# Optimization experiments

Measured on AMD Instinct MI355X. Metric: run time of the kernel, lower is better.

The kernel has to match this reference:

```python
import jax, jax.numpy as jnp
import numpy as np

# Config (matches init_kwargs)
L = 2        # depth
DIM = 512
H = 8        # heads
DH = 64      # dim_head
MLP = 2048
B = 4
N = 1024
BLOCK = 32   # compress / selection block size
TOPK = 8     # num_selected_blocks
WRAD = 32    # sliding window radius (window size 64)


def setup_inputs() -> dict:
    key = jax.random.key(0)
    ks = jax.random.split(key, 10)
    s = 0.02
    def rn(k, shape):
        return jax.random.normal(k, shape, dtype=jnp.float32) * s
    return {
        "x": jax.random.normal(ks[0], (B, N, DIM), dtype=jnp.float32),
        "ln1_g": jnp.ones((L, DIM), jnp.float32), "ln1_b": jnp.zeros((L, DIM), jnp.float32),
        "Wq": rn(ks[1], (L, DIM, H * DH)), "Wk": rn(ks[2], (L, DIM, H * DH)), "Wv": rn(ks[3], (L, DIM, H * DH)),
        "Wg": rn(ks[4], (L, DIM, H * 3)), "bg": jnp.zeros((L, H * 3), jnp.float32),
        "Wo": rn(ks[5], (L, H * DH, DIM)), "bo": jnp.zeros((L, DIM), jnp.float32),
        "ln2_g": jnp.ones((L, DIM), jnp.float32), "ln2_b": jnp.zeros((L, DIM), jnp.float32),
        "W1": rn(ks[6], (L, DIM, MLP)), "b1": jnp.zeros((L, MLP), jnp.float32),
        "W2": rn(ks[7], (L, MLP, DIM)), "b2": jnp.zeros((L, DIM), jnp.float32),
    }


def _ln(x, g, b):
    m = x.mean(-1, keepdims=True)
    v = jnp.var(x, axis=-1, keepdims=True)
    return (x - m) * jax.lax.rsqrt(v + 1e-5) * g + b


def _sparse_attn(x, lng, lnb, Wq, Wk, Wv, Wg, bg, Wo, bo):
    # NSA-style 3-branch attention: compressed + selected-blocks + sliding window,
    # combined with per-head sigmoid gates. Non-causal (ViT).
    b, n, _ = x.shape
    h = _ln(x, lng, lnb)
    q = (h @ Wq).reshape(b, n, H, DH).transpose(0, 2, 1, 3)  # bhnd
    k = (h @ Wk).reshape(b, n, H, DH).transpose(0, 2, 1, 3)
    v = (h @ Wv).reshape(b, n, H, DH).transpose(0, 2, 1, 3)
    q = q * (DH ** -0.5)
    nb = n // BLOCK
    # --- compressed branch: mean-pool K/V per block
    kc = k.reshape(b, H, nb, BLOCK, DH).mean(3)              # bhmd (m = nb blocks)
    vc = v.reshape(b, H, nb, BLOCK, DH).mean(3)
    sc = jnp.einsum('bhnd,bhmd->bhnm', q, kc)                # per-query block scores
    out_c = jnp.einsum('bhnm,bhmd->bhnd', jax.nn.softmax(sc, -1), vc)
    # --- selection branch: top-k blocks per query (from compressed scores)
    idx = jax.lax.top_k(sc, TOPK)[1]                         # [b,h,n,TOPK]
    blk_mask = (idx[..., :, None] == jnp.arange(nb)).any(-2) # [b,h,n,nb]
    tok_mask = jnp.repeat(blk_mask, BLOCK, axis=-1)          # [b,h,n,n]
    s = jnp.einsum('bhnd,bhmd->bhnm', q, k)                  # shared fine scores
    neg = jnp.finfo(s.dtype).min
    out_s = jnp.einsum('bhnm,bhmd->bhnd',
                       jax.nn.softmax(jnp.where(tok_mask, s, neg), -1), v)
    # --- sliding window branch
    i = jnp.arange(n)
    wmask = jnp.abs(i[:, None] - i[None, :]) <= WRAD
    out_w = jnp.einsum('bhnm,bhmd->bhnd',
                       jax.nn.softmax(jnp.where(wmask, s, neg), -1), v)
    # --- gate and combine
    gates = jax.nn.sigmoid(h @ Wg + bg).reshape(b, n, H, 3).transpose(0, 2, 1, 3)[..., None]  # [b,H,n,3,1]
    out = gates[:, :, :, 0] * out_c + gates[:, :, :, 1] * out_s + gates[:, :, :, 2] * out_w
    out = out.transpose(0, 2, 1, 3).reshape(b, n, H * DH)
    return out @ Wo + bo


def reference(x, ln1_g, ln1_b, Wq, Wk, Wv, Wg, bg, Wo, bo, ln2_g, ln2_b, W1, b1, W2, b2):
    for l in range(L):
        x = _sparse_attn(x, ln1_g[l], ln1_b[l], Wq[l], Wk[l], Wv[l],
                         Wg[l], bg[l], Wo[l], bo[l]) + x
        h = _ln(x, ln2_g[l], ln2_b[l])
        x = jax.nn.gelu(h @ W1[l] + b1[l]) @ W2[l] + b2[l] + x
    return x
```

## Files before the change

kernel.cpp:

```cpp
#include <hip/hip_runtime.h>
#include <cstdint>
#include <cstddef>

typedef __attribute__((ext_vector_type(4))) float f32x4;
typedef __attribute__((ext_vector_type(16))) float f32x16;
typedef __attribute__((ext_vector_type(8))) short short8;
typedef __attribute__((ext_vector_type(4))) short s16x4;
typedef __attribute__((ext_vector_type(2))) int int2v;
typedef unsigned short u16;

#define DEVINL static __device__ __forceinline__
#define MFMA32(A,B,C) __builtin_amdgcn_mfma_f32_32x32x16_bf16(A,B,C,0,0,0)

constexpr int NBATCH = 4;
constexpr int NSEQ   = 1024;
constexpr int NDIM   = 512;
constexpr int NHEAD  = 8;
constexpr int NDH    = 64;
constexpr int NMLP   = 2048;
constexpr int NROWS  = NBATCH * NSEQ;
constexpr int NBLKC  = 32;
constexpr int NBH    = NBATCH * NHEAD;
constexpr int NQKV   = 1664;

DEVINL float b2f(u16 u) { union { unsigned u; float f; } x; x.u = ((unsigned)u) << 16; return x.f; }
DEVINL u16 f2b(float v) {
    union { float f; unsigned u; } x; x.f = v;
    unsigned r = x.u + 0x7fff + ((x.u >> 16) & 1);
    return (u16)(r >> 16);
}
DEVINL float fastrcp(float x) { float r; asm("v_rcp_f32 %0, %1" : "=v"(r) : "v"(x)); return r; }

DEVINL void gload16(const void* g, void* l)
{
    __builtin_amdgcn_global_load_lds(
        (const __attribute__((address_space(1))) void*)g,
        (__attribute__((address_space(3))) void*)l, 16, 0, 0);
}

__global__ void __launch_bounds__(256) ln_kernel(const float* __restrict__ x,
    const float* __restrict__ gg, const float* __restrict__ bb, u16* __restrict__ out)
{
    int row = blockIdx.x * 4 + (threadIdx.x >> 6);
    int lane = threadIdx.x & 63;
    const float* xr = x + (size_t)row * NDIM + lane * 8;
    f32x4 a = *(const f32x4*)xr;
    f32x4 c = *(const f32x4*)(xr + 4);
    float xv[8] = { a[0], a[1], a[2], a[3], c[0], c[1], c[2], c[3] };
    float s = 0.f, s2 = 0.f;
    #pragma unroll
    for (int i = 0; i < 8; ++i) { s += xv[i]; s2 += xv[i] * xv[i]; }
    #pragma unroll
    for (int d = 1; d < 64; d <<= 1) { s += __shfl_xor(s, d); s2 += __shfl_xor(s2, d); }
    float mean = s * (1.f / NDIM);
    float var = s2 * (1.f / NDIM) - mean * mean;
    float rstd = rsqrtf(var + 1e-5f);
    const float* gp = gg + lane * 8;
    const float* bp = bb + lane * 8;
    short8 o;
    #pragma unroll
    for (int i = 0; i < 8; ++i)
        o[i] = (short)f2b((xv[i] - mean) * rstd * gp[i] + bp[i]);
    *(short8*)(out + (size_t)row * NDIM + lane * 8) = o;
}

__global__ void __launch_bounds__(256) setup_weights(
    const float* __restrict__ Wq, const float* __restrict__ Wk, const float* __restrict__ Wv,
    const float* __restrict__ Wg, const float* __restrict__ Wo,
    const float* __restrict__ W1, const float* __restrict__ W2,
    u16* __restrict__ wqkvT, u16* __restrict__ woT,
    u16* __restrict__ w1T, u16* __restrict__ w2T)
{
    int j = blockIdx.x;
    if (j >= 6144) {
        int j5 = j - 6144, l = j5 >> 2, chunk = j5 & 3;
        u16* d2 = wqkvT + (size_t)l * NQKV * 512 + (size_t)(1536 + chunk * 32) * 512;
        const float* src = Wg + (size_t)l * 512 * 24;
        for (int e = threadIdx.x; e < 16384; e += 256) {
            int r = chunk * 32 + (e >> 9), k = e & 511;
            d2[(size_t)(e >> 9) * 512 + k] = (r < 24) ? f2b(src[(size_t)k * 24 + r]) : (u16)0;
        }
        return;
    }
    __shared__ float tile[32][33];
    const float* W; u16* dst; int K, Nc, bx, by;
    if (j < 1536) {
        int z = j >> 8, t = j & 255, l = z / 3, wsel = z % 3;
        W = (wsel == 0 ? Wq : (wsel == 1 ? Wk : Wv)) + (size_t)l * 262144;
        dst = wqkvT + (size_t)l * NQKV * 512 + (size_t)wsel * 262144;
        K = 512; Nc = 512; bx = t & 15; by = t >> 4;
    } else if (j < 2048) {
        int j2 = j - 1536, z = j2 >> 8, t = j2 & 255;
        W = Wo + (size_t)z * 262144; dst = woT + (size_t)z * 262144;
        K = 512; Nc = 512; bx = t & 15; by = t >> 4;
    } else if (j < 4096) {
        int j3 = j - 2048, z = j3 >> 10, t = j3 & 1023;
        W = W1 + (size_t)z * 1048576; dst = w1T + (size_t)z * 1048576;
        K = 512; Nc = 2048; bx = t & 63; by = t >> 6;
    } else {
        int j4 = j - 4096, z = j4 >> 10, t = j4 & 1023;
        W = W2 + (size_t)z * 1048576; dst = w2T + (size_t)z * 1048576;
        K = 2048; Nc = 512; bx = t & 15; by = t >> 4;
    }
    int tx = threadIdx.x & 31, ty = threadIdx.x >> 5;
    int n0 = bx * 32, k0 = by * 32;
    #pragma unroll
    for (int r = 0; r < 4; ++r)
        tile[ty * 4 + r][tx] = W[(size_t)(k0 + ty * 4 + r) * Nc + n0 + tx];
    __syncthreads();
    #pragma unroll
    for (int r = 0; r < 4; ++r)
        dst[(size_t)(n0 + ty * 4 + r) * K + k0 + tx] = f2b(tile[tx][ty * 4 + r]);
}

enum { EP_QKV = 0, EP_GELU = 1, EP_RES = 2 };

template<int BM, int BN, int BK, int KT, int EPIL>
__global__ void __launch_bounds__(256) gemm_k(
    const u16* __restrict__ A, const u16* __restrict__ BT,
    int M, int Nc,
    const float* __restrict__ bias,
    float* __restrict__ resout,
    u16* __restrict__ outb,
    u16* __restrict__ q16, u16* __restrict__ k16, u16* __restrict__ vt16,
    u16* __restrict__ kc16 = nullptr, u16* __restrict__ vct16 = nullptr)
{
    constexpr int NT = KT / BK;
    constexpr int NK = BK / 32;
    constexpr int RB = BK * 2;
    constexpr int RMSK = (BK == 64) ? 7 : 3;
    constexpr int LA = BM * BK / 2048;
    constexpr int LBD = BN * BK / 2048;
    constexpr int LB = LA + LBD;
    constexpr int WM = BM / 2, WN = BN / 2;
    constexpr int MI = WM / 16, NI = WN / 16;
    __shared__ u16 As[3][BM][BK];
    __shared__ u16 Bs[3][BN][BK];
    const int tid = threadIdx.x;
    const int lane = tid & 63;
    const int wid = tid >> 6;
    const int wm = wid >> 1, wn = wid & 1;
    const int gx = gridDim.x;
    const int nblk = gx * gridDim.y;
    const int id = blockIdx.y * gx + blockIdx.x;
    const int sid = (id & 7) * (nblk >> 3) + (id >> 3);
    const int rowBase = (sid / gx) * BM;
    const int colBase = (sid % gx) * BN;
    const int fr = lane & 15;
    const int kg = lane >> 4;

    auto stage = [&](int buf, int t) {
        const size_t k0 = (size_t)t * BK;
        char* aL = (char*)&As[buf][0][0];
        #pragma unroll
        for (int p = 0; p < LA; ++p) {
            int idx = p * 256 + tid;
            int row = idx / (BK / 8);
            int ob = (idx % (BK / 8)) * 16;
            int sw = ob ^ ((row & RMSK) << 4);
            gload16((const char*)(A + (size_t)(rowBase + row) * KT + k0) + sw, aL + idx * 16);
        }
        char* bL = (char*)&Bs[buf][0][0];
        #pragma unroll
        for (int p = 0; p < LBD; ++p) {
            int idx = p * 256 + tid;
            int row = idx / (BK / 8);
            int ob = (idx % (BK / 8)) * 16;
            int sw = ob ^ ((row & RMSK) << 4);
            gload16((const char*)(BT + (size_t)(colBase + row) * KT + k0) + sw, bL + idx * 16);
        }
    };

    stage(0, 0);
    stage(1, 1);
    f32x4 acc[MI][NI] = {};
    int cb = 0, nb = 1, sb = 2;
    for (int t = 0; t < NT; ++t) {
        if (t == NT - 1) asm volatile("s_waitcnt vmcnt(0)" ::: "memory");
        else             asm volatile("s_waitcnt vmcnt(%0)" :: "n"(LB) : "memory");
        __builtin_amdgcn_s_barrier();
        if (t + 2 < NT) stage(sb, t + 2);
        const char* aB = (const char*)&As[cb][0][0];
        const char* bB = (const char*)&Bs[cb][0][0];
        #pragma unroll
        for (int kk = 0; kk < NK; ++kk) {
            short8 af[MI], bfr[NI];
            #pragma unroll
            for (int i = 0; i < MI; ++i) {
                int row = wm * WM + i * 16 + fr;
                af[i] = *(const short8*)(aB + row * RB + ((kk * 64 + kg * 16) ^ ((row & RMSK) << 4)));
            }
            #pragma unroll
            for (int j = 0; j < NI; ++j) {
                int row = wn * WN + j * 16 + fr;
                bfr[j] = *(const short8*)(bB + row * RB + ((kk * 64 + kg * 16) ^ ((row & RMSK) << 4)));
            }
            #pragma unroll
            for (int i = 0; i < MI; ++i)
                #pragma unroll
                for (int j = 0; j < NI; ++j)
                    acc[i][j] = __builtin_amdgcn_mfma_f32_16x16x32_bf16(af[i], bfr[j], acc[i][j], 0, 0, 0);
        }
        int tmp = cb; cb = nb; nb = sb; sb = tmp;
    }

    #pragma unroll
    for (int i = 0; i < MI; ++i) {
        #pragma unroll
        for (int j = 0; j < NI; ++j) {
            int col = colBase + wn * WN + j * 16 + fr;
            if constexpr (EPIL == EP_QKV) {
                int which = col >> 9;
                int row0 = rowBase + wm * WM + i * 16 + kg * 4;
                if (which >= 3) {
                    int c2 = col - 1536;
                    if (c2 < 24) {
                        #pragma unroll
                        for (int rr = 0; rr < 4; ++rr) {
                            float xg = acc[i][j][rr] + bias[c2];
                            resout[(size_t)(row0 + rr) * 24 + c2] =
                                fastrcp(1.f + exp2f(-1.4426950409f * xg));
                        }
                    }
                } else {
                    int c = col & 511;
                    int hh = c >> 6, dh = c & 63;
                    int bb2 = row0 >> 10, n0 = row0 & 1023;
                    size_t bh2 = (size_t)(bb2 * NHEAD + hh) * 65536;
                    if (which == 2) {
                        s16x4 pk;
                        #pragma unroll
                        for (int rr = 0; rr < 4; ++rr) pk[rr] = (short)f2b(acc[i][j][rr]);
                        *(s16x4*)&vt16[bh2 + (size_t)dh * NSEQ + n0] = pk;
                    } else {
                        u16* dst = (which ? k16 : q16) + bh2 + (size_t)n0 * NDH + dh;
                        float scl = which ? 1.f : 0.18033688f;
                        #pragma unroll
                        for (int rr = 0; rr < 4; ++rr) dst[rr * NDH] = f2b(acc[i][j][rr] * scl);
                    }
                }
            } else {
                #pragma unroll
                for (int rr = 0; rr < 4; ++rr) {
                    int row = rowBase + wm * WM + i * 16 + kg * 4 + rr;
                    float val = acc[i][j][rr];
                    if constexpr (EPIL == EP_GELU) {
                        float t = val + bias[col];
                        float u = t + 0.044715f * t * t * t;
                        float gs = fastrcp(1.f + exp2f(-2.3022083f * u));
                        outb[(size_t)row * Nc + col] = f2b(t * gs);
                    } else {
                        resout[(size_t)row * Nc + col] += val + bias[col];
                    }
                }
            }
        }
    }

    if constexpr (EPIL == EP_QKV) {
        const int m = ((rowBase & 1023) >> 5) + wm;
        const int bb2 = rowBase >> 10;
        #pragma unroll
        for (int j = 0; j < NI; ++j) {
            int col = colBase + wn * WN + j * 16 + fr;
            int which = col >> 9;
            if (which == 1 || which == 2) {
                float ps = 0.f;
                #pragma unroll
                for (int i = 0; i < MI; ++i)
                    #pragma unroll
                    for (int rr = 0; rr < 4; ++rr) ps += acc[i][j][rr];
                ps += __shfl_xor(ps, 16);
                ps += __shfl_xor(ps, 32);
                if (kg == 0) {
                    int c = col & 511, hh = c >> 6, dh = c & 63;
                    size_t bhp = (size_t)(bb2 * NHEAD + hh) * 2048;
                    float mval = ps * (1.f / 32.f);
                    if (which == 1) kc16[bhp + m * 64 + dh] = f2b(mval);
                    else            vct16[bhp + (size_t)dh * 32 + m] = f2b(mval);
                }
            }
        }
    }
}

DEVINL unsigned cvtpk(float lo, float hi_)
{
    unsigned t;
    asm("v_cvt_pk_bf16_f32 %0, %1, %2" : "=v"(t) : "v"(lo), "v"(hi_));
    return t;
}

DEVINL void plswap(unsigned& a, unsigned& b)
{
#if __has_builtin(__builtin_amdgcn_permlane32_swap)
    int2v r = __builtin_amdgcn_permlane32_swap((int)a, (int)b, false, false);
    a = (unsigned)r[0]; b = (unsigned)r[1];
#else
    asm("v_permlane32_swap_b32 %0, %1" : "+v"(a), "+v"(b));
#endif
}

DEVINL void packswap(const float* e, unsigned selmask, short8& pb0, short8& pb1)
{
    unsigned w[8];
    #pragma unroll
    for (int i = 0; i < 8; ++i) w[i] = cvtpk(e[2 * i], e[2 * i + 1]) & selmask;
    plswap(w[0], w[2]); plswap(w[1], w[3]);
    plswap(w[4], w[6]); plswap(w[5], w[7]);
    union { unsigned u[4]; short8 s; } c0, c1;
    c0.u[0] = w[0]; c0.u[1] = w[1]; c0.u[2] = w[2]; c0.u[3] = w[3];
    c1.u[0] = w[4]; c1.u[1] = w[5]; c1.u[2] = w[6]; c1.u[3] = w[7];
    pb0 = c0.s; pb1 = c1.s;
}

template<int R0>
DEVINL unsigned rank4(const f32x16& sc_, const float* po, int hi)
{
    unsigned bits = 0;
    #pragma unroll
    for (int k = 0; k < 4; ++k) {
        const int r = R0 + k;
        const int krr = (r & 3) + 8 * (r >> 2);
        const float sr = sc_[r];
        int cnt = 0;
        #pragma unroll
        for (int j = 0; j < 16; ++j) {
            const int krj = (j & 3) + 8 * (j >> 2);
            if (j != r) cnt += (sc_[j] > sr || (sc_[j] == sr && krj < krr)) ? 1 : 0;
            const bool pless = (hi == 0) ? (krj + 4 < krr) : (krj < krr + 4);
            cnt += (po[j] > sr || (po[j] == sr && pless)) ? 1 : 0;
        }
        if (cnt < 8) bits |= 1u << (krr + 4 * hi);
    }
    return bits;
}

__global__ void __launch_bounds__(256, 2) attn_mfma(
    const u16* __restrict__ qb, const u16* __restrict__ kb, const u16* __restrict__ vt,
    const u16* __restrict__ kc16, const u16* __restrict__ vct16,
    const float* __restrict__ gates, u16* __restrict__ att)
{
    __shared__ __align__(16) char smem[65536];
    unsigned* selb_lds = (unsigned*)(smem + 32768);
    const int tid = threadIdx.x;
    const int wid = tid >> 6;
    const int lane = tid & 63;
    const int qc = lane & 31, hi = lane >> 5;
    const int g = blockIdx.x;
    const int xcd = g & 7, ii = g >> 3;
    const int bh = xcd * 4 + (ii >> 5);
    const int qt = ii & 31;
    const int qrow = qt * 32 + qc;
    if (tid < 32) selb_lds[tid] = 0u;
    const u16* Q = qb + (size_t)bh * 65536;
    const char* Kby = (const char*)(kb + (size_t)bh * 65536);
    const char* Vby = (const char*)(vt + (size_t)bh * 65536);

    const int l16 = lane * 16;
    auto stage = [&](int buf, int blk) {
        char* base = smem + buf * 32768 + wid * 4096;
        #pragma unroll
        for (int i = 0; i < 4; ++i) {
            int o = i * 1024 + l16;
            int so = o ^ (((o >> 7) & 7) << 4);
            gload16(Kby + (size_t)blk * 4096 + so, base + o);
        }
        #pragma unroll
        for (int i = 0; i < 4; ++i) {
            int o = i * 1024 + l16;
            int row = o >> 6;
            int colb = (o & 63) ^ ((row & 3) << 4);
            gload16(Vby + (size_t)row * 2048 + blk * 64 + colb, base + 16384 + o);
        }
    };
    const int blo = wid * 8;
    stage(0, blo);

    short8 qf[4];
    #pragma unroll
    for (int ks = 0; ks < 4; ++ks)
        qf[ks] = *(const short8*)&Q[(size_t)qrow * 64 + ks * 16 + hi * 8];
    const int b = bh >> 3, h = bh & 7;
    const float* grow = gates + (size_t)(b * 1024 + qrow) * 24 + h * 3;
    const float g0 = grow[0], g1 = grow[1], g2 = grow[2];

    const u16* Kc = kc16 + (size_t)bh * 2048;
    const u16* Vc = vct16 + (size_t)bh * 2048;
    f32x16 sc_ = {};
    #pragma unroll
    for (int ks = 0; ks < 4; ++ks) {
        short8 kcf = *(const short8*)&Kc[qc * 64 + ks * 16 + hi * 8];
        sc_ = MFMA32(kcf, qf[ks], sc_);
    }
    float po[16];
    #pragma unroll
    for (int r = 0; r < 16; ++r) po[r] = __shfl_xor(sc_[r], 32);
    unsigned bits;
    switch (wid) {
        case 0:  bits = rank4<0>(sc_, po, hi); break;
        case 1:  bits = rank4<4>(sc_, po, hi); break;
        case 2:  bits = rank4<8>(sc_, po, hi); break;
        default: bits = rank4<12>(sc_, po, hi); break;
    }
    __syncthreads();
    atomicOr(&selb_lds[qc], bits);

    f32x16 aC = {};
    float denc = 1.f;
    if (wid < 2) {
        float ec[16]; float dsum = 0.f;
        #pragma unroll
        for (int r = 0; r < 16; ++r) { ec[r] = exp2f(sc_[r]); dsum += ec[r]; }
        denc = dsum + __shfl_xor(dsum, 32);
        short8 pc0, pc1;
        packswap(ec, 0xFFFFFFFFu, pc0, pc1);
        const u16* Vch = Vc + (wid * 32 + qc) * 32 + hi * 8;
        short8 vcA = *(const short8*)&Vch[0];
        short8 vcB = *(const short8*)&Vch[16];
        aC = MFMA32(vcA, pc0, aC);
        aC = MFMA32(vcB, pc1, aC);
    }
    __syncthreads();
    const unsigned mask = selb_lds[qc];

    f32x16 aS0 = {}, aS1 = {}, aW0 = {}, aW1 = {};
    float denS = 0.f, denW = 0.f;
    const int wlo = qt > 0 ? qt - 1 : 0;
    const int whi = qt < 31 ? qt + 1 : 31;

    int kra[4];
    #pragma unroll
    for (int ks = 0; ks < 4; ++ks)
        kra[ks] = wid * 4096 + ((qc * 128 + ks * 32 + hi * 16) ^ ((qc & 7) << 4));
    const int vbase = wid * 4096 + 16384;
    const int v00o = vbase + ((qc * 64 + hi * 16) ^ ((qc & 3) << 4));
    const int v01o = vbase + ((qc * 64 + 32 + hi * 16) ^ ((qc & 3) << 4));
    const int v10o = vbase + ((2048 + qc * 64 + hi * 16) ^ ((qc & 3) << 4));
    const int v11o = vbase + ((2048 + qc * 64 + 32 + hi * 16) ^ ((qc & 3) << 4));

    for (int t = 0; t < 8; ++t) {
        const int blk = blo + t;
        const char* base = smem + (t & 1) * 32768;
        if (t < 7) {
            stage((t + 1) & 1, blk + 1);
            asm volatile("s_waitcnt vmcnt(8)" ::: "memory");
        } else {
            asm volatile("s_waitcnt vmcnt(0)" ::: "memory");
        }
        short8 kf[4];
        #pragma unroll
        for (int ks = 0; ks < 4; ++ks)
            kf[ks] = *(const short8*)(base + kra[ks]);
        __builtin_amdgcn_s_setprio(1);
        f32x16 s = {};
        #pragma unroll
        for (int ks = 0; ks < 4; ++ks)
            s = MFMA32(kf[ks], qf[ks], s);
        __builtin_amdgcn_s_setprio(0);
        float e[16];
        #pragma unroll
        for (int r = 0; r < 16; ++r) e[r] = exp2f(s[r]);

        short8 v00 = *(const short8*)(base + v00o);
        short8 v01 = *(const short8*)(base + v01o);
        short8 v10 = *(const short8*)(base + v10o);
        short8 v11 = *(const short8*)(base + v11o);

        const bool selb = (mask >> blk) & 1u;
        const unsigned selm = selb ? 0xFFFFFFFFu : 0u;
        {
            float tt = 0.f;
            #pragma unroll
            for (int r = 0; r < 16; ++r) tt += e[r];
            denS += selb ? tt : 0.f;
        }
        short8 pb0, pb1;
        packswap(e, selm, pb0, pb1);
        __builtin_amdgcn_s_setprio(1);
        aS0 = MFMA32(v00, pb0, aS0);
        aS0 = MFMA32(v01, pb1, aS0);
        aS1 = MFMA32(v10, pb0, aS1);
        aS1 = MFMA32(v11, pb1, aS1);
        __builtin_amdgcn_s_setprio(0);

        if (blk >= wlo && blk <= whi) {
            float ew[16];
            float tt = 0.f;
            #pragma unroll
            for (int r = 0; r < 16; ++r) {
                int kr = (r & 3) + 8 * (r >> 2) + 4 * hi;
                int dd = blk * 32 + kr - qrow;
                ew[r] = (dd >= -32 && dd <= 32) ? e[r] : 0.f;
                tt += ew[r];
            }
            denW += tt;
            short8 pw0, pw1;
            packswap(ew, 0xFFFFFFFFu, pw0, pw1);
            aW0 = MFMA32(v00, pw0, aW0);
            aW0 = MFMA32(v01, pw1, aW0);
            aW1 = MFMA32(v10, pw0, aW1);
            aW1 = MFMA32(v11, pw1, aW1);
        }
    }
    __syncthreads();

    float* cmb = (float*)smem;
    if (wid > 0) {
        float* dst = cmb + (size_t)(wid - 1) * (64 * 85) + lane * 85;
        #pragma unroll
        for (int i = 0; i < 16; ++i) { dst[i] = aS0[i]; dst[16 + i] = aS1[i]; }
        #pragma unroll
        for (int i = 0; i < 16; ++i) { dst[32 + i] = aW0[i]; dst[48 + i] = aW1[i]; }
        dst[64] = denS; dst[65] = denW;
        if (wid == 1) {
            #pragma unroll
            for (int i = 0; i < 16; ++i) dst[66 + i] = aC[i];
        }
    }
    __syncthreads();
    if (wid == 0) {
        #pragma unroll
        for (int w = 1; w < 4; ++w) {
            const float* src = cmb + (size_t)(w - 1) * (64 * 85) + lane * 85;
            #pragma unroll
            for (int i = 0; i < 16; ++i) { aS0[i] += src[i]; aS1[i] += src[16 + i]; }
            #pragma unroll
            for (int i = 0; i < 16; ++i) { aW0[i] += src[32 + i]; aW1[i] += src[48 + i]; }
            denS += src[64]; denW += src[65];
        }
        f32x16 aC1;
        const float* s1 = cmb + lane * 85;
        #pragma unroll
        for (int i = 0; i < 16; ++i) aC1[i] = s1[66 + i];
        denS += __shfl_xor(denS, 32);
        denW += __shfl_xor(denW, 32);
        const float rc = g0 / denc, rs = g1 / denS, rw = g2 / denW;
        u16* op = att + (size_t)(b * 1024 + qrow) * NDIM + h * 64;
        #pragma unroll
        for (int c4 = 0; c4 < 4; ++c4) {
            int d0 = c4 * 8 + hi * 4;
            s16x4 w0, w1;
            #pragma unroll
            for (int j = 0; j < 4; ++j) {
                w0[j] = (short)f2b(rc * aC[c4 * 4 + j]  + rs * aS0[c4 * 4 + j] + rw * aW0[c4 * 4 + j]);
                w1[j] = (short)f2b(rc * aC1[c4 * 4 + j] + rs * aS1[c4 * 4 + j] + rw * aW1[c4 * 4 + j]);
            }
            *(s16x4*)&op[d0] = w0;
            *(s16x4*)&op[d0 + 32] = w1;
        }
    }
}

extern "C" void kernel_launch(void* const* d_in, const int* in_sizes, int n_in,
                              void* d_out, int out_size, void* d_ws, size_t ws_size,
                              hipStream_t stream)
{
    const float* x0    = (const float*)d_in[0];
    const float* ln1_g = (const float*)d_in[1];
    const float* ln1_b = (const float*)d_in[2];
    const float* Wq    = (const float*)d_in[3];
    const float* Wk    = (const float*)d_in[4];
    const float* Wv    = (const float*)d_in[5];
    const float* Wg    = (const float*)d_in[6];
    const float* bg    = (const float*)d_in[7];
    const float* Wo    = (const float*)d_in[8];
    const float* bo    = (const float*)d_in[9];
    const float* ln2_g = (const float*)d_in[10];
    const float* ln2_b = (const float*)d_in[11];
    const float* W1    = (const float*)d_in[12];
    const float* b1    = (const float*)d_in[13];
    const float* W2    = (const float*)d_in[14];
    const float* b2    = (const float*)d_in[15];
    float* xo = (float*)d_out;

    char* w = (char*)d_ws;
    auto alloc = [&](size_t bytes) { char* p = w; w += (bytes + 255) & ~(size_t)255; return p; };
    u16*   hbf   = (u16*)  alloc((size_t)NROWS * NDIM * 2);
    u16*   qb    = (u16*)  alloc((size_t)NBH * NSEQ * NDH * 2);
    u16*   kb    = (u16*)  alloc((size_t)NBH * NSEQ * NDH * 2);
    u16*   vt    = (u16*)  alloc((size_t)NBH * NDH * NSEQ * 2);
    u16*   att   = (u16*)  alloc((size_t)NROWS * NDIM * 2);
    float* gates = (float*)alloc((size_t)NROWS * NHEAD * 3 * 4);
    u16*   kc16  = (u16*)  alloc((size_t)NBH * NBLKC * NDH * 2);
    u16*   vct16 = (u16*)  alloc((size_t)NBH * NDH * NBLKC * 2);
    u16*   wqkvT = (u16*)  alloc((size_t)2 * NQKV * 512 * 2);
    u16*   woT   = (u16*)  alloc((size_t)2 * 512 * 512 * 2);
    u16*   w1T   = (u16*)  alloc((size_t)2 * 2048 * 512 * 2);
    u16*   w2T   = (u16*)  alloc((size_t)2 * 512 * 2048 * 2);
    u16*   mid   = (u16*)qb;

    hipMemcpyAsync(xo, x0, (size_t)NROWS * NDIM * 4, hipMemcpyDeviceToDevice, stream);

    setup_weights<<<6152, 256, 0, stream>>>(Wq, Wk, Wv, Wg, Wo, W1, W2, wqkvT, woT, w1T, w2T);

    for (int l = 0; l < 2; ++l) {
        ln_kernel<<<NROWS / 4, 256, 0, stream>>>(xo, ln1_g + l * NDIM, ln1_b + l * NDIM, hbf);
        gemm_k<64, 128, 64, 512, EP_QKV><<<dim3(NQKV / 128, NROWS / 64), 256, 0, stream>>>(
            hbf, wqkvT + (size_t)l * NQKV * 512, NROWS, NQKV,
            bg + l * 24, gates, nullptr, qb, kb, vt, kc16, vct16);
        attn_mfma<<<1024, 256, 0, stream>>>(qb, kb, vt, kc16, vct16, gates, att);
        gemm_k<64, 64, 64, 512, EP_RES><<<dim3(512 / 64, NROWS / 64), 256, 0, stream>>>(
            att, woT + (size_t)l * 512 * 512, NROWS, 512,
            bo + l * NDIM, xo, nullptr, nullptr, nullptr, nullptr);
        ln_kernel<<<NROWS / 4, 256, 0, stream>>>(xo, ln2_g + l * NDIM, ln2_b + l * NDIM, hbf);
        gemm_k<64, 128, 64, 512, EP_GELU><<<dim3(2048 / 128, NROWS / 64), 256, 0, stream>>>(
            hbf, w1T + (size_t)l * 2048 * 512, NROWS, 2048,
            b1 + l * NMLP, nullptr, mid, nullptr, nullptr, nullptr);
        gemm_k<64, 64, 64, 2048, EP_RES><<<dim3(512 / 64, NROWS / 64), 256, 0, stream>>>(
            mid, w2T + (size_t)l * 512 * 2048, NROWS, 512,
            b2 + l * NDIM, xo, nullptr, nullptr, nullptr, nullptr);
    }
}
```

Measured before the change: 240.6 us.

## Restructure attention LDS staging to triple-buffer K/V and shrink shared memory

Each wave now keeps two K buffers and one V buffer (12 KB per wave instead of 16 KB double-buffered). K is prefetched two blocks ahead, V one block ahead, and the V fragments are read into registers before the next load is issued. Total LDS drops from 64 KB to 48 KB, and the cross-wave reduction is serialized through a single swizzled payload region. The aim is more occupancy headroom and earlier loads, at the cost of extra barriers in the reduction and a redundant clamped K load at the tail.

```diff
diff --git a/kernel.cpp b/kernel.cpp
--- a/kernel.cpp
+++ b/kernel.cpp
@@ -341,12 +341,13 @@
     const u16* __restrict__ kc16, const u16* __restrict__ vct16,
     const float* __restrict__ gates, u16* __restrict__ att)
 {
-    __shared__ __align__(16) char smem[65536];
-    unsigned* selb_lds = (unsigned*)(smem + 32768);
+    __shared__ __align__(16) char smem[49152];
+    __shared__ unsigned selb_lds[32];
     const int tid = threadIdx.x;
     const int wid = tid >> 6;
     const int lane = tid & 63;
     const int qc = lane & 31, hi = lane >> 5;
+    const int lm = lane & 31;
     const int g = blockIdx.x;
     const int xcd = g & 7, ii = g >> 3;
     const int bh = xcd * 4 + (ii >> 5);
@@ -358,24 +359,29 @@
     const char* Vby = (const char*)(vt + (size_t)bh * 65536);
 
     const int l16 = lane * 16;
-    auto stage = [&](int buf, int blk) {
-        char* base = smem + buf * 32768 + wid * 4096;
+    auto stageK = [&](int kbuf, int blk) {
+        char* base = smem + wid * 12288 + kbuf * 4096;
         #pragma unroll
         for (int i = 0; i < 4; ++i) {
             int o = i * 1024 + l16;
             int so = o ^ (((o >> 7) & 7) << 4);
             gload16(Kby + (size_t)blk * 4096 + so, base + o);
         }
+    };
+    auto stageV = [&](int blk) {
+        char* base = smem + wid * 12288 + 8192;
         #pragma unroll
         for (int i = 0; i < 4; ++i) {
             int o = i * 1024 + l16;
             int row = o >> 6;
             int colb = (o & 63) ^ ((row & 3) << 4);
-            gload16(Vby + (size_t)row * 2048 + blk * 64 + colb, base + 16384 + o);
+            gload16(Vby + (size_t)row * 2048 + blk * 64 + colb, base + o);
         }
     };
     const int blo = wid * 8;
-    stage(0, blo);
+    stageK(0, blo);
+    stageV(blo);
+    stageK(1, blo + 1);
 
     short8 qf[4];
     #pragma unroll
@@ -432,8 +438,8 @@
     int kra[4];
     #pragma unroll
     for (int ks = 0; ks < 4; ++ks)
-        kra[ks] = wid * 4096 + ((qc * 128 + ks * 32 + hi * 16) ^ ((qc & 7) << 4));
-    const int vbase = wid * 4096 + 16384;
+        kra[ks] = wid * 12288 + ((qc * 128 + ks * 32 + hi * 16) ^ ((qc & 7) << 4));
+    const int vbase = wid * 12288 + 8192;
     const int v00o = vbase + ((qc * 64 + hi * 16) ^ ((qc & 3) << 4));
     const int v01o = vbase + ((qc * 64 + 32 + hi * 16) ^ ((qc & 3) << 4));
     const int v10o = vbase + ((2048 + qc * 64 + hi * 16) ^ ((qc & 3) << 4));
@@ -441,17 +447,21 @@
 
     for (int t = 0; t < 8; ++t) {
         const int blk = blo + t;
-        const char* base = smem + (t & 1) * 32768;
+        asm volatile("s_waitcnt vmcnt(4)" ::: "memory");
+        const char* kbase = smem + ((t & 1) << 12);
+        short8 kf[4];
+        #pragma unroll
+        for (int ks = 0; ks < 4; ++ks)
+            kf[ks] = *(const short8*)(kbase + kra[ks]);
+        short8 v00 = *(const short8*)(smem + v00o);
+        short8 v01 = *(const short8*)(smem + v01o);
+        short8 v10 = *(const short8*)(smem + v10o);
+        short8 v11 = *(const short8*)(smem + v11o);
         if (t < 7) {
-            stage((t + 1) & 1, blk + 1);
-            asm volatile("s_waitcnt vmcnt(8)" ::: "memory");
-        } else {
-            asm volatile("s_waitcnt vmcnt(0)" ::: "memory");
-        }
-        short8 kf[4];
-        #pragma unroll
-        for (int ks = 0; ks < 4; ++ks)
-            kf[ks] = *(const short8*)(base + kra[ks]);
+            asm volatile("s_waitcnt lgkmcnt(0)" ::: "memory");
+            stageV(blk + 1);
+            stageK(t & 1, blk + 2 <= 31 ? blk + 2 : 31);
+        }
         __builtin_amdgcn_s_setprio(1);
         f32x16 s = {};
         #pragma unroll
@@ -461,11 +471,6 @@
         float e[16];
         #pragma unroll
         for (int r = 0; r < 16; ++r) e[r] = exp2f(s[r]);
-
-        short8 v00 = *(const short8*)(base + v00o);
-        short8 v01 = *(const short8*)(base + v01o);
-        short8 v10 = *(const short8*)(base + v10o);
-        short8 v11 = *(const short8*)(base + v11o);
 
         const bool selb = (mask >> blk) & 1u;
         const unsigned selm = selb ? 0xFFFFFFFFu : 0u;
@@ -503,36 +508,45 @@
             aW1 = MFMA32(v11, pw1, aW1);
         }
     }
+    asm volatile("s_waitcnt vmcnt(0)" ::: "memory");
     __syncthreads();
 
-    float* cmb = (float*)smem;
-    if (wid > 0) {
-        float* dst = cmb + (size_t)(wid - 1) * (64 * 85) + lane * 85;
-        #pragma unroll
-        for (int i = 0; i < 16; ++i) { dst[i] = aS0[i]; dst[16 + i] = aS1[i]; }
-        #pragma unroll
-        for (int i = 0; i < 16; ++i) { dst[32 + i] = aW0[i]; dst[48 + i] = aW1[i]; }
-        dst[64] = denS; dst[65] = denW;
-        if (wid == 1) {
-            #pragma unroll
-            for (int i = 0; i < 16; ++i) dst[66 + i] = aC[i];
-        }
-    }
-    __syncthreads();
+    float* pay = (float*)smem;
+    f32x16 aC1 = {};
+    #define SW(s) (((s) & ~31) | (((s) & 31) ^ lm))
+    for (int w = 1; w < 4; ++w) {
+        if (wid == w) {
+            float* d = pay + (size_t)lane * 128;
+            #pragma unroll
+            for (int i = 0; i < 16; ++i) { d[SW(i)] = aS0[i]; d[SW(16 + i)] = aS1[i]; }
+            #pragma unroll
+            for (int i = 0; i < 16; ++i) { d[SW(32 + i)] = aW0[i]; d[SW(48 + i)] = aW1[i]; }
+            d[97] = denW;
+            if (w == 1) {
+                #pragma unroll
+                for (int i = 0; i < 16; ++i) d[SW(64 + i)] = aC[i];
+            }
+            d[96] = denS;
+        }
+        __syncthreads();
+        if (wid == 0) {
+            const float* sr = pay + (size_t)lane * 128;
+            #pragma unroll
+            for (int i = 0; i < 16; ++i) { aS0[i] += sr[SW(i)]; aS1[i] += sr[SW(16 + i)]; }
+            denS += sr[96];
+            #pragma unroll
+            for (int i = 0; i < 16; ++i) { aW0[i] += sr[SW(32 + i)]; aW1[i] += sr[SW(48 + i)]; }
+            denW += sr[97];
+            if (w == 1) {
+                #pragma unroll
+                for (int i = 0; i < 16; ++i) aC1[i] = sr[SW(64 + i)];
+            }
+        }
+        __syncthreads();
+    }
+    #undef SW
+
     if (wid == 0) {
-        #pragma unroll
-        for (int w = 1; w < 4; ++w) {
-            const float* src = cmb + (size_t)(w - 1) * (64 * 85) + lane * 85;
-            #pragma unroll
-            for (int i = 0; i < 16; ++i) { aS0[i] += src[i]; aS1[i] += src[16 + i]; }
-            #pragma unroll
-            for (int i = 0; i < 16; ++i) { aW0[i] += src[32 + i]; aW1[i] += src[48 + i]; }
-            denS += src[64]; denW += src[65];
-        }
-        f32x16 aC1;
-        const float* s1 = cmb + lane * 85;
-        #pragma unroll
-        for (int i = 0; i < 16; ++i) aC1[i] = s1[66 + i];
         denS += __shfl_xor(denS, 32);
         denW += __shfl_xor(denW, 32);
         const float rc = g0 / denc, rs = g1 / denS, rw = g2 / denW;
```

After: 245.1 us. About the same (+1.9%).
